# Performance work log

Hardware: AMD Instinct MI355X
Metric: run time of the kernel (lower is better)

Reference implementation:

```python
import jax, jax.numpy as jnp
import numpy as np

BN_EPS = 1e-5


def _conv(x, w, b):
    # x [B,C,H,W], w [O,I,kh,kw], VALID padding, stride 1
    out = jax.lax.conv_general_dilated(x, w, (1, 1), 'VALID',
                                       dimension_numbers=('NCHW', 'OIHW', 'NCHW'))
    return out + b[None, :, None, None]


def _bilinear(img, y, x):
    # img [B,C,H,W]; y,x [B,K,Ho,Wo] fractional sample coords; zero outside.
    B, C, H, W = img.shape
    y0 = jnp.floor(y); x0 = jnp.floor(x)
    y1 = y0 + 1.0;     x1 = x0 + 1.0
    wy1 = y - y0; wy0 = 1.0 - wy1
    wx1 = x - x0; wx0 = 1.0 - wx1
    bidx = jnp.arange(B)[:, None, None, None]

    def g(yi, xi, wgt):
        valid = (yi >= 0) & (yi <= H - 1) & (xi >= 0) & (xi <= W - 1)
        yc = jnp.clip(yi, 0, H - 1).astype(jnp.int32)
        xc = jnp.clip(xi, 0, W - 1).astype(jnp.int32)
        v = img[bidx, :, yc, xc]  # [B,K,Ho,Wo,C]
        return v * (wgt * valid)[..., None]

    return (g(y0, x0, wy0 * wx0) + g(y0, x1, wy0 * wx1)
            + g(y1, x0, wy1 * wx0) + g(y1, x1, wy1 * wx1))


def _dcn_out(x, w_off, b_off, w_dcn, b_dcn, gamma, beta):
    k = w_dcn.shape[2]          # kernel height (kernel = (k,1))
    pad = k // 2
    # F.pad([0,0,pad,pad]): pad H only
    xp = jnp.pad(x, ((0, 0), (0, 0), (pad, pad), (0, 0)))
    B, C, Hp, W = xp.shape
    Ho = Hp - k + 1             # == original H for odd k
    Wo = W
    # offset/mask conv: 3*k output channels (dy | dx | mask)
    om = _conv(xp, w_off, b_off)                  # [B,3k,Ho,Wo]
    dy, dx = om[:, :k], om[:, k:2 * k]
    mask = jax.nn.sigmoid(om[:, 2 * k:])          # [B,k,Ho,Wo]
    # sample coordinates: base grid + per-tap offset
    y = (jnp.arange(Ho, dtype=x.dtype)[None, None, :, None]
         + jnp.arange(k, dtype=x.dtype)[None, :, None, None] + dy)
    xc = jnp.arange(Wo, dtype=x.dtype)[None, None, None, :] + dx
    sampled = _bilinear(xp, y, xc) * mask[..., None]   # [B,k,Ho,Wo,C]
    out = jnp.einsum('bkhwc,ock->bohw', sampled, w_dcn[:, :, :, 0])
    out = out + b_dcn[None, :, None, None]
    # BatchNorm2d (training-mode batch statistics) + ReLU
    mean = out.mean(axis=(0, 2, 3), keepdims=True)
    var = out.var(axis=(0, 2, 3), keepdims=True)
    out = (out - mean) * jax.lax.rsqrt(var + BN_EPS)
    out = out * gamma[None, :, None, None] + beta[None, :, None, None]
    return jax.nn.relu(out)


def setup_inputs() -> dict:
    key = jax.random.key(0)
    ks = jax.random.split(key, 6)
    B, C, H, W, k = 8, 64, 256, 256, 3
    x = jax.random.normal(ks[0], (B, C, H, W), dtype=jnp.float32)
    fan = C * k
    w_off = jax.random.normal(ks[1], (3 * k, C, k, 1), dtype=jnp.float32) * 0.01
    b_off = jnp.zeros((3 * k,), dtype=jnp.float32)
    w_dcn = jax.random.normal(ks[2], (C, C, k, 1), dtype=jnp.float32) / np.sqrt(fan)
    b_dcn = jax.random.normal(ks[3], (C,), dtype=jnp.float32) * 0.01
    gamma = jnp.ones((C,), dtype=jnp.float32)
    beta = jnp.zeros((C,), dtype=jnp.float32)
    return {'x': x, 'w_off': w_off, 'b_off': b_off, 'w_dcn': w_dcn,
            'b_dcn': b_dcn, 'gamma': gamma, 'beta': beta}


def reference(x, w_off, b_off, w_dcn, b_dcn, gamma, beta):
    return _dcn_out(x, w_off, b_off, w_dcn, b_dcn, gamma, beta)
```

## Files before the change

### kernel.cpp

```cpp
#include <hip/hip_runtime.h>
#include <cmath>

#define HW 65536
#define NPER 524288
#define NBLK 8192

typedef _Float16 f16;
typedef __attribute__((ext_vector_type(8))) _Float16 f16x8;
typedef __attribute__((ext_vector_type(4))) _Float16 f16x4;
typedef __attribute__((ext_vector_type(4))) float f32x4;

__device__ __forceinline__ f16x8 splat8(f16 h) {
  f16x8 r = {h, h, h, h, h, h, h, h};
  return r;
}

#define SUMS_OFF  0
#define WTO_OFF   128
#define WTH_OFF   1664
#define PART_OFF  7808
#define XT_OFF    1056384
#define OUT16_OFF 17833600

__global__ __launch_bounds__(256) void prep_wts(
    const float* __restrict__ w_off, const float* __restrict__ w_dcn,
    f16* __restrict__ wtO, f16* __restrict__ wtH, float* __restrict__ sums) {
  int i = blockIdx.x * 256 + threadIdx.x;
  if (i < 128) sums[i] = 0.f;
  if (i < 12288) {
    int o = i / 192, k = i - o * 192, kh = k >> 6, c = k & 63;
    wtH[i] = (f16)w_dcn[(o * 64 + c) * 3 + kh];
  }
  if (i < 3072) {
    int n = i / 192, k = i - n * 192, kh = k >> 6, c = k & 63;
    wtO[i] = (n < 9) ? (f16)w_off[(n * 64 + c) * 3 + kh] : (f16)0.f;
  }
}

__global__ __launch_bounds__(256) void xpose(
    const float* __restrict__ x, f16* __restrict__ xT) {
  __shared__ f16 sX[64 * 68];
  int t = threadIdx.x, lane = t & 63, cq = t >> 6;
  int blk = blockIdx.x;
  int b = blk >> 10;
  int rem = blk & 1023;
  int h = rem >> 2, w0 = (rem & 3) << 6;
  int c0 = cq << 4;
  const float* xb = x + (((size_t)b) << 6) * HW + (size_t)h * 256 + w0 + lane;
  float v[16];
#pragma unroll
  for (int j = 0; j < 16; ++j) v[j] = xb[(size_t)(c0 + j) * HW];
  f16x8 a, bb;
#pragma unroll
  for (int j = 0; j < 8; ++j) { a[j] = (f16)v[j]; bb[j] = (f16)v[8 + j]; }
  f16* d = sX + lane * 68 + c0;
  *(f16x8*)d = a;
  *(f16x8*)(d + 8) = bb;
  __syncthreads();
  int px = t >> 2, c16 = (t & 3) << 4;
  f16x8 o0 = *(const f16x8*)(sX + px * 68 + c16);
  f16x8 o1 = *(const f16x8*)(sX + px * 68 + c16 + 8);
  f16* dst = xT + (((size_t)b * HW + (size_t)h * 256 + w0 + px) << 6) + c16;
  *(f16x8*)dst = o0;
  *(f16x8*)(dst + 8) = o1;
}

__global__ __launch_bounds__(256, 5) void dcn_fused(
    const f16* __restrict__ xT, const f16* __restrict__ wtO,
    const float* __restrict__ b_off, const f16* __restrict__ wtH,
    const float* __restrict__ b_dcn, f16* __restrict__ out16,
    float* __restrict__ part) {
  __shared__ __align__(16) unsigned char lds[30208];
  f16*   sA   = (f16*)lds;
  float* sOut = (float*)lds;
  float* sOM  = (float*)(lds + 25600);
  unsigned short* sWo = (unsigned short*)(lds + 25600);
  f16*   sWw  = (f16*)(lds + 27136);
  float* sP   = (float*)(lds + 27136);

  const int t = threadIdx.x, lane = t & 63, cq = t >> 6;
  const int c0 = cq << 4;
  const int lrow = lane & 15, lq = lane >> 4, kgrp = lq << 3;
  const int pix8 = lane >> 3, chunk = lane & 7;
  const int cb8 = chunk << 3;

  int g = ((blockIdx.x & 7) << 10) | (blockIdx.x >> 3);
  int b = g >> 10;
  int rem = g & 1023;
  int h = rem >> 2, w0 = (rem & 3) << 6;
  const f16* xb = xT + (((size_t)b * HW) << 6);

  f16x8 Ac[6];
#pragma unroll
  for (int kt = 0; kt < 6; ++kt) {
    int hr = h + (kt >> 1) - 1;
    int hc = min(max(hr, 0), 255);
    int cb = ((kt & 1) << 5) + kgrp;
    const f16* src = xb + (((size_t)(hc * 256 + w0 + c0 + lrow)) << 6) + cb;
    f16x8 v = *(const f16x8*)src;
    if (!(hr >= 0 && hr < 256)) v = splat8((f16)0.f);
    Ac[kt] = v;
  }
  f32x4 accO = {0.f, 0.f, 0.f, 0.f};
#pragma unroll
  for (int kt = 0; kt < 6; ++kt) {
    f16x8 Bo = *(const f16x8*)(wtO + lrow * 192 + kt * 32 + kgrp);
    accO = __builtin_amdgcn_mfma_f32_16x16x32_f16(Ac[kt], Bo, accO, 0, 0, 0);
  }
  float boffv = (lrow < 9) ? b_off[lrow] : 0.f;
#pragma unroll
  for (int r = 0; r < 4; ++r)
    sOM[(c0 + lq * 4 + r) * 17 + lrow] = accO[r] + boffv;
  __syncthreads();

  float dy = 0.f, dxv = 0.f, mpre = 0.f;
  int px = t & 63, khw = t >> 6;
  if (t < 192) {
    dy   = sOM[px * 17 + khw];
    dxv  = sOM[px * 17 + 3 + khw];
    mpre = sOM[px * 17 + 6 + khw];
  }
  __syncthreads();
  if (t < 192) {
    float m = 1.f / (1.f + __expf(-mpre));
    float yf = (float)(h + khw) + dy;
    float xf = (float)(w0 + px) + dxv;
    float y0f = floorf(yf), x0f = floorf(xf);
    int iy0 = (int)y0f, ix0 = (int)x0f;
    float wy1 = yf - y0f, wy0 = 1.f - wy1;
    float wx1 = xf - x0f, wx0 = 1.f - wx1;
    int r0 = iy0 - 1, r1 = iy0, g0 = ix0, g1 = ix0 + 1;
    bool vr0 = (r0 >= 0) & (r0 < 256), vr1 = (r1 >= 0) & (r1 < 256);
    bool vc0 = (g0 >= 0) & (g0 < 256), vc1 = (g1 >= 0) & (g1 < 256);
    float w00 = (vr0 & vc0) ? wy0 * wx0 * m : 0.f;
    float w01 = (vr0 & vc1) ? wy0 * wx1 * m : 0.f;
    float w10 = (vr1 & vc0) ? wy1 * wx0 * m : 0.f;
    float w11 = (vr1 & vc1) ? wy1 * wx1 * m : 0.f;
    int e = px * 3 + khw;
    sWo[e * 4 + 0] = (unsigned short)min(max(r0, 0), 255);
    sWo[e * 4 + 1] = (unsigned short)min(max(r1, 0), 255);
    sWo[e * 4 + 2] = (unsigned short)min(max(g0, 0), 255);
    sWo[e * 4 + 3] = (unsigned short)min(max(g1, 0), 255);
    sWw[e * 4 + 0] = (f16)w00;
    sWw[e * 4 + 1] = (f16)w01;
    sWw[e * 4 + 2] = (f16)w10;
    sWw[e * 4 + 3] = (f16)w11;
  }
  __syncthreads();

  ushort4 po[6];
  f16x4  wv[6];
#pragma unroll
  for (int i = 0; i < 6; ++i) {
    int kh = i >> 1, half = i & 1;
    int e = (c0 + half * 8 + pix8) * 3 + kh;
    po[i] = *(const ushort4*)(sWo + e * 4);
    wv[i] = *(const f16x4*)(sWw + e * 4);
  }
  f16x8 gv[24];
#pragma unroll
  for (int i = 0; i < 6; ++i) {
    int b00 = (((int)po[i].x << 8) + (int)po[i].z) << 6;
    int b01 = (((int)po[i].x << 8) + (int)po[i].w) << 6;
    int b10 = (((int)po[i].y << 8) + (int)po[i].z) << 6;
    int b11 = (((int)po[i].y << 8) + (int)po[i].w) << 6;
    gv[i * 4 + 0] = *(const f16x8*)(xb + b00 + cb8);
    gv[i * 4 + 1] = *(const f16x8*)(xb + b01 + cb8);
    gv[i * 4 + 2] = *(const f16x8*)(xb + b10 + cb8);
    gv[i * 4 + 3] = *(const f16x8*)(xb + b11 + cb8);
  }
#pragma unroll
  for (int i = 0; i < 6; ++i) {
    int kh = i >> 1, half = i & 1;
    f16x8 s = gv[i * 4 + 0] * splat8(wv[i][0]) +
              gv[i * 4 + 1] * splat8(wv[i][1]) +
              gv[i * 4 + 2] * splat8(wv[i][2]) +
              gv[i * 4 + 3] * splat8(wv[i][3]);
    *(f16x8*)(sA + (c0 + half * 8 + pix8) * 200 + kh * 64 + cb8) = s;
  }

  const int nrow = c0 + lrow;
  f16x8 Bf[6];
#pragma unroll
  for (int kt = 0; kt < 6; ++kt)
    Bf[kt] = *(const f16x8*)(wtH + nrow * 192 + kt * 32 + kgrp);
  float bdc = b_dcn[nrow];
  __syncthreads();

  f32x4 acc[4];
#pragma unroll
  for (int mt = 0; mt < 4; ++mt) acc[mt] = (f32x4){0.f, 0.f, 0.f, 0.f};
#pragma unroll
  for (int kt = 0; kt < 6; ++kt) {
#pragma unroll
    for (int mt = 0; mt < 4; ++mt) {
      f16x8 Af = *(const f16x8*)(sA + (mt * 16 + lrow) * 200 + kt * 32 + kgrp);
      acc[mt] = __builtin_amdgcn_mfma_f32_16x16x32_f16(Af, Bf[kt], acc[mt],
                                                       0, 0, 0);
    }
  }
  __syncthreads();

  float s1 = 0.f, s2 = 0.f;
#pragma unroll
  for (int mt = 0; mt < 4; ++mt) {
    int prow = mt * 16 + lq * 4;
    f32x4 vv;
#pragma unroll
    for (int r = 0; r < 4; ++r) {
      float v = acc[mt][r] + bdc;
      vv[r] = v;
      s1 += v;
      s2 += v * v;
    }
    *(f32x4*)(sOut + nrow * 66 + prow) = vv;
  }
  s1 += __shfl_xor(s1, 16); s1 += __shfl_xor(s1, 32);
  s2 += __shfl_xor(s2, 16); s2 += __shfl_xor(s2, 32);
  if (lq == 0) {
    sP[nrow] = s1;
    sP[64 + nrow] = s2;
  }
  __syncthreads();

  if (t < 128) part[(size_t)blockIdx.x * 128 + t] = sP[t];
  f16* ob = out16 + (((size_t)b) << 6) * HW + (size_t)h * 256 + w0;
#pragma unroll
  for (int i = 0; i < 16; ++i) {
    int o = c0 + i;
    ob[(size_t)o * HW + lane] = (f16)sOut[o * 66 + lane];
  }
}

__global__ __launch_bounds__(256) void reduce_sums(
    const float* __restrict__ part, float* __restrict__ sums) {
  int r = blockIdx.x;
  int j = threadIdx.x & 127, half = threadIdx.x >> 7;
  const float* p = part + ((size_t)r * 64 + half * 32) * 128 + j;
  float s = 0.f;
#pragma unroll
  for (int i = 0; i < 32; ++i) s += p[(size_t)i * 128];
  __shared__ float ls[256];
  ls[threadIdx.x] = s;
  __syncthreads();
  if (threadIdx.x < 128)
    atomicAdd(&sums[threadIdx.x], ls[threadIdx.x] + ls[128 + threadIdx.x]);
}

__global__ __launch_bounds__(256) void bn_apply(
    const f16* __restrict__ out16, float* __restrict__ out,
    const float* __restrict__ sums, const float* __restrict__ gamma,
    const float* __restrict__ beta) {
  int blk = blockIdx.x;
  int pl = blk >> 2, q = blk & 3;
  int o = pl & 63;
  float mean = sums[o] * (1.f / (float)NPER);
  float var = sums[64 + o] * (1.f / (float)NPER) - mean * mean;
  float inv = rsqrtf(var + 1e-5f);
  float sc = gamma[o] * inv;
  float sh = beta[o] - mean * sc;
  const f16x8* src = (const f16x8*)(out16 + (size_t)pl * HW + q * 16384);
  float4* dst = (float4*)(out + (size_t)pl * HW + q * 16384);
  for (int i = threadIdx.x; i < 2048; i += 256) {
    f16x8 v = src[i];
    float4 lo, hi;
    lo.x = fmaxf(fmaf((float)v[0], sc, sh), 0.f);
    lo.y = fmaxf(fmaf((float)v[1], sc, sh), 0.f);
    lo.z = fmaxf(fmaf((float)v[2], sc, sh), 0.f);
    lo.w = fmaxf(fmaf((float)v[3], sc, sh), 0.f);
    hi.x = fmaxf(fmaf((float)v[4], sc, sh), 0.f);
    hi.y = fmaxf(fmaf((float)v[5], sc, sh), 0.f);
    hi.z = fmaxf(fmaf((float)v[6], sc, sh), 0.f);
    hi.w = fmaxf(fmaf((float)v[7], sc, sh), 0.f);
    dst[2 * i] = lo;
    dst[2 * i + 1] = hi;
  }
}

extern "C" void kernel_launch(void* const* d_in, const int* in_sizes, int n_in,
                              void* d_out, int out_size, void* d_ws, size_t ws_size,
                              hipStream_t stream) {
  const float* x     = (const float*)d_in[0];
  const float* w_off = (const float*)d_in[1];
  const float* b_off = (const float*)d_in[2];
  const float* w_dcn = (const float*)d_in[3];
  const float* b_dcn = (const float*)d_in[4];
  const float* gamma = (const float*)d_in[5];
  const float* beta  = (const float*)d_in[6];
  float* out = (float*)d_out;
  float* ws  = (float*)d_ws;

  float* sums = ws + SUMS_OFF;
  f16*   wtO  = (f16*)(ws + WTO_OFF);
  f16*   wtH  = (f16*)(ws + WTH_OFF);
  float* part = ws + PART_OFF;
  f16*   xT   = (f16*)(ws + XT_OFF);
  f16*   o16  = (f16*)(ws + OUT16_OFF);

  prep_wts<<<48, 256, 0, stream>>>(w_off, w_dcn, wtO, wtH, sums);
  xpose<<<8192, 256, 0, stream>>>(x, xT);
  dcn_fused<<<NBLK, 256, 0, stream>>>(xT, wtO, b_off, wtH, b_dcn, o16, part);
  reduce_sums<<<128, 256, 0, stream>>>(part, sums);
  bn_apply<<<2048, 256, 0, stream>>>(o16, out, sums, gamma, beta);
}
```

Before: 375.1 us.

## Vectorize transpose loads and output stores, shrink LDS for higher occupancy

The transpose kernel now has each thread load float4 runs along W for one channel instead of scalar strided loads. In the fused DCN kernel the LDS regions are overlapped so shared memory drops from about 30KB to 25.6KB, and launch bounds rise to 6 blocks per SM. One barrier is removed, the weight-fragment loads are hoisted ahead of the sampling writes, and the fp16 output stores are packed as f16x4. The reuse of overlapping LDS regions relies on the barrier placement staying correct, and the scalar fp16 LDS writes in the transpose may cause bank conflicts.

```diff
diff --git a/kernel.cpp b/kernel.cpp
--- a/kernel.cpp
+++ b/kernel.cpp
@@ -40,22 +40,25 @@
 __global__ __launch_bounds__(256) void xpose(
     const float* __restrict__ x, f16* __restrict__ xT) {
   __shared__ f16 sX[64 * 68];
-  int t = threadIdx.x, lane = t & 63, cq = t >> 6;
+  int t = threadIdx.x;
   int blk = blockIdx.x;
   int b = blk >> 10;
   int rem = blk & 1023;
   int h = rem >> 2, w0 = (rem & 3) << 6;
-  int c0 = cq << 4;
-  const float* xb = x + (((size_t)b) << 6) * HW + (size_t)h * 256 + w0 + lane;
-  float v[16];
-#pragma unroll
-  for (int j = 0; j < 16; ++j) v[j] = xb[(size_t)(c0 + j) * HW];
-  f16x8 a, bb;
-#pragma unroll
-  for (int j = 0; j < 8; ++j) { a[j] = (f16)v[j]; bb[j] = (f16)v[8 + j]; }
-  f16* d = sX + lane * 68 + c0;
-  *(f16x8*)d = a;
-  *(f16x8*)(d + 8) = bb;
+  int c = t >> 2, w4 = t & 3;
+  const float* xb = x + (((size_t)b << 6) + c) * HW + (size_t)h * 256 + w0;
+  float4 v[4];
+#pragma unroll
+  for (int i = 0; i < 4; ++i)
+    v[i] = *(const float4*)(xb + ((w4 + 4 * i) << 2));
+#pragma unroll
+  for (int i = 0; i < 4; ++i) {
+    int w = (w4 + 4 * i) << 2;
+    sX[(w + 0) * 68 + c] = (f16)v[i].x;
+    sX[(w + 1) * 68 + c] = (f16)v[i].y;
+    sX[(w + 2) * 68 + c] = (f16)v[i].z;
+    sX[(w + 3) * 68 + c] = (f16)v[i].w;
+  }
   __syncthreads();
   int px = t >> 2, c16 = (t & 3) << 4;
   f16x8 o0 = *(const f16x8*)(sX + px * 68 + c16);
@@ -65,18 +68,18 @@
   *(f16x8*)(dst + 8) = o1;
 }
 
-__global__ __launch_bounds__(256, 5) void dcn_fused(
+__global__ __launch_bounds__(256, 6) void dcn_fused(
     const f16* __restrict__ xT, const f16* __restrict__ wtO,
     const float* __restrict__ b_off, const f16* __restrict__ wtH,
     const float* __restrict__ b_dcn, f16* __restrict__ out16,
     float* __restrict__ part) {
-  __shared__ __align__(16) unsigned char lds[30208];
+  __shared__ __align__(16) unsigned char lds[25600];
   f16*   sA   = (f16*)lds;
+  float* sOM  = (float*)lds;
+  unsigned short* sWo = (unsigned short*)(lds + 4352);
+  f16*   sWw  = (f16*)(lds + 5888);
   float* sOut = (float*)lds;
-  float* sOM  = (float*)(lds + 25600);
-  unsigned short* sWo = (unsigned short*)(lds + 25600);
-  f16*   sWw  = (f16*)(lds + 27136);
-  float* sP   = (float*)(lds + 27136);
+  float* sP   = (float*)(lds + 16896);
 
   const int t = threadIdx.x, lane = t & 63, cq = t >> 6;
   const int c0 = cq << 4;
@@ -113,15 +116,11 @@
     sOM[(c0 + lq * 4 + r) * 17 + lrow] = accO[r] + boffv;
   __syncthreads();
 
-  float dy = 0.f, dxv = 0.f, mpre = 0.f;
   int px = t & 63, khw = t >> 6;
   if (t < 192) {
-    dy   = sOM[px * 17 + khw];
-    dxv  = sOM[px * 17 + 3 + khw];
-    mpre = sOM[px * 17 + 6 + khw];
-  }
-  __syncthreads();
-  if (t < 192) {
+    float dy   = sOM[px * 17 + khw];
+    float dxv  = sOM[px * 17 + 3 + khw];
+    float mpre = sOM[px * 17 + 6 + khw];
     float m = 1.f / (1.f + __expf(-mpre));
     float yf = (float)(h + khw) + dy;
     float xf = (float)(w0 + px) + dxv;
@@ -169,6 +168,14 @@
     gv[i * 4 + 2] = *(const f16x8*)(xb + b10 + cb8);
     gv[i * 4 + 3] = *(const f16x8*)(xb + b11 + cb8);
   }
+  const int nrow = c0 + lrow;
+  f16x8 Bf[6];
+#pragma unroll
+  for (int kt = 0; kt < 6; ++kt)
+    Bf[kt] = *(const f16x8*)(wtH + nrow * 192 + kt * 32 + kgrp);
+  float bdc = b_dcn[nrow];
+  __syncthreads();
+
 #pragma unroll
   for (int i = 0; i < 6; ++i) {
     int kh = i >> 1, half = i & 1;
@@ -178,13 +185,6 @@
               gv[i * 4 + 3] * splat8(wv[i][3]);
     *(f16x8*)(sA + (c0 + half * 8 + pix8) * 200 + kh * 64 + cb8) = s;
   }
-
-  const int nrow = c0 + lrow;
-  f16x8 Bf[6];
-#pragma unroll
-  for (int kt = 0; kt < 6; ++kt)
-    Bf[kt] = *(const f16x8*)(wtH + nrow * 192 + kt * 32 + kgrp);
-  float bdc = b_dcn[nrow];
   __syncthreads();
 
   f32x4 acc[4];
@@ -225,10 +225,15 @@
 
   if (t < 128) part[(size_t)blockIdx.x * 128 + t] = sP[t];
   f16* ob = out16 + (((size_t)b) << 6) * HW + (size_t)h * 256 + w0;
-#pragma unroll
-  for (int i = 0; i < 16; ++i) {
-    int o = c0 + i;
-    ob[(size_t)o * HW + lane] = (f16)sOut[o * 66 + lane];
+  const int eo = lane >> 4, ew = (lane & 15) << 2;
+#pragma unroll
+  for (int i = 0; i < 4; ++i) {
+    int o = c0 + i * 4 + eo;
+    const float* sr = sOut + o * 66 + ew;
+    f16x4 pk;
+    pk[0] = (f16)sr[0]; pk[1] = (f16)sr[1];
+    pk[2] = (f16)sr[2]; pk[3] = (f16)sr[3];
+    *(f16x4*)(ob + (size_t)o * HW + ew) = pk;
   }
 }
 
```

Result: slower. 388.8 us (+3.6%).
